# Optimization experiments

Measured on AMD Instinct MI355X. Metric: run time of the kernel, lower is better.

The kernel has to match this reference:

```python
import jax, jax.numpy as jnp
import numpy as np

B, L, D = 2, 2048, 2048
H, KV, HD = 16, 8, 128
EPS = 1e-5
ROPE_BASE = 10000.0
SCALING_ALPHA = 1.0
SCALE = HD ** -0.5


def setup_inputs() -> dict:
    key = jax.random.key(0)
    ks = jax.random.split(key, 5)
    s = 0.02  # weight init scale
    return {
        "x": jax.random.normal(ks[0], (B, L, D), jnp.float32),
        "wq": jax.random.normal(ks[1], (D, H * HD), jnp.float32) * s,
        "wk": jax.random.normal(ks[2], (D, KV * HD), jnp.float32) * s,
        "wv": jax.random.normal(ks[3], (D, KV * HD), jnp.float32) * s,
        "wo": jax.random.normal(ks[4], (H * HD, D), jnp.float32) * s,
        "qn_w": jnp.ones((HD,), jnp.float32),
        "kn_w": jnp.ones((HD,), jnp.float32),
    }


def _rope(t):
    # t: [B, h, L, HD]. DynamicNTKAlpha base scaling (alpha=1 -> no-op).
    base = ROPE_BASE * SCALING_ALPHA ** (HD / (HD - 2))
    # NOTE: source uses base**(+i/d) (no negative exponent) -- kept faithful.
    freqs = base ** (jnp.arange(0, HD, 2, dtype=jnp.float32) / HD)  # [HD/2]
    pos = jnp.arange(t.shape[-2], dtype=jnp.float32)                # [L]
    angles = pos[:, None] * freqs[None, :]                          # [L, HD/2]
    cos, sin = jnp.cos(angles), jnp.sin(angles)
    x1, x2 = t[..., : HD // 2], t[..., HD // 2 :]
    return jnp.concatenate([x1 * cos - x2 * sin, x2 * cos + x1 * sin], axis=-1)


def _rmsnorm(t, w):
    return t * jax.lax.rsqrt(jnp.mean(t * t, axis=-1, keepdims=True) + EPS) * w


def reference(x, wq, wk, wv, wo, qn_w, kn_w):
    b, l, _ = x.shape
    q = (x @ wq).reshape(b, l, H, HD).transpose(0, 2, 1, 3)   # [B,H,L,HD]
    k = (x @ wk).reshape(b, l, KV, HD).transpose(0, 2, 1, 3)  # [B,KV,L,HD]
    v = (x @ wv).reshape(b, l, KV, HD).transpose(0, 2, 1, 3)
    q = _rmsnorm(_rope(q), qn_w)
    k = _rmsnorm(_rope(k), kn_w)
    # GQA: expand KV heads to match query heads
    rep = H // KV
    k = jnp.repeat(k, rep, axis=1)  # [B,H,L,HD]
    v = jnp.repeat(v, rep, axis=1)
    scores = jnp.einsum("bhqd,bhkd->bhqk", q, k) * SCALE
    probs = jax.nn.softmax(scores, axis=-1)
    out = jnp.einsum("bhqk,bhkd->bhqd", probs, v)             # [B,H,L,HD]
    out = out.transpose(0, 2, 1, 3).reshape(b, l, H * HD)
    return out @ wo
```

## Files before the change

kernel.cpp:

```cpp
#include <hip/hip_runtime.h>
#include <math.h>

#define BB 2
#define LL 2048
#define DD 2048
#define HH 16
#define KVH 8
#define HDIM 128
#define SCALE_F 0.08838834764831845f
#define EPS_F 1e-5f
#define LOG2E 1.4426950408889634f
#define SMAX_F 17.0f
#define QKVW 4096

typedef unsigned short u16;
typedef __attribute__((ext_vector_type(8))) short short8;
typedef __attribute__((ext_vector_type(4))) float f32x4;

#define MFMA16(a, b, c) __builtin_amdgcn_mfma_f32_16x16x32_bf16((a), (b), (c), 0, 0, 0)

__device__ __forceinline__ float b2f(u16 u) {
    union { unsigned int i; float f; } x;
    x.i = ((unsigned int)u) << 16;
    return x.f;
}
__device__ __forceinline__ u16 f2b(float f) {
    unsigned int x = __float_as_uint(f);
    unsigned int r = x + 0x7FFFu + ((x >> 16) & 1u);
    return (u16)(r >> 16);
}
__device__ __forceinline__ u16 f2b_fast(float f) {
    return (u16)((__float_as_uint(f) + 0x8000u) >> 16);
}
__device__ __forceinline__ void g2l(const u16* g, u16* l) {
    __builtin_amdgcn_global_load_lds(
        (const __attribute__((address_space(1))) unsigned int*)g,
        (__attribute__((address_space(3))) unsigned int*)l, 16, 0, 0);
}

__global__ __launch_bounds__(256) void convert_f32_bf16(const float* __restrict__ in,
                                                        u16* __restrict__ out, int n) {
    int i = (blockIdx.x * 256 + threadIdx.x) * 4;
    if (i >= n) return;
    float4 v = *(const float4*)(in + i);
    unsigned int p0 = (unsigned int)f2b(v.x) | ((unsigned int)f2b(v.y) << 16);
    unsigned int p1 = (unsigned int)f2b(v.z) | ((unsigned int)f2b(v.w) << 16);
    uint2 pk; pk.x = p0; pk.y = p1;
    *(uint2*)(out + i) = pk;
}

__global__ __launch_bounds__(256) void transpose_conv(const float* __restrict__ in,
                                                      u16* __restrict__ out, int R, int C) {
    __shared__ u16 t[64 * 65];
    int c0 = blockIdx.x * 64, r0 = blockIdx.y * 64;
#pragma unroll
    for (int i = 0; i < 16; i++) {
        int idx = threadIdx.x + i * 256;
        int r = idx >> 6, c = idx & 63;
        t[r * 65 + c] = f2b(in[(size_t)(r0 + r) * C + c0 + c]);
    }
    __syncthreads();
#pragma unroll
    for (int i = 0; i < 16; i++) {
        int idx = threadIdx.x + i * 256;
        int r = idx >> 6, c = idx & 63;
        out[(size_t)(c0 + r) * R + r0 + c] = t[c * 65 + r];
    }
}

__global__ __launch_bounds__(256) void transpose_v(const u16* __restrict__ qkv,
                                                   u16* __restrict__ vt) {
    __shared__ u16 t[64 * 65];
    int l0 = blockIdx.x * 64, d0 = blockIdx.y * 64;
    int bg = blockIdx.z, b = bg >> 3, g = bg & 7;
    const u16* src = qkv + (size_t)b * LL * QKVW + 3072 + g * HDIM;
    u16* dst = vt + (size_t)bg * HDIM * LL;
#pragma unroll
    for (int i = 0; i < 16; i++) {
        int idx = threadIdx.x + i * 256;
        int r = idx >> 6, c = idx & 63;
        t[r * 65 + c] = src[(size_t)(l0 + r) * QKVW + d0 + c];
    }
    __syncthreads();
#pragma unroll
    for (int i = 0; i < 16; i++) {
        int idx = threadIdx.x + i * 256;
        int r = idx >> 6, c = idx & 63;
        dst[(size_t)(d0 + r) * LL + l0 + c] = t[c * 65 + r];
    }
}

__global__ __launch_bounds__(256) void rope_table(float* __restrict__ ct, float* __restrict__ st) {
    int i = blockIdx.x * 256 + threadIdx.x;
    int pos = i >> 6, d = i & 63;
    float freq = (float)pow(10000.0, (double)d * (1.0 / 64.0));
    float ang = (float)pos * freq;
    double a = (double)ang;
    ct[i] = (float)cos(a);
    st[i] = (float)sin(a);
}

template <bool F32OUT>
__global__ __launch_bounds__(256) void gemm_bt(const u16* __restrict__ A,
                                               const u16* __restrict__ Bt,
                                               void* __restrict__ Cv, int M, int N, int K) {
    __shared__ __align__(16) u16 As[128 * 32];
    __shared__ __align__(16) u16 Bs[128 * 32];
    const int tid = threadIdx.x;
    const int w = tid >> 6, lane = tid & 63;
    const int lm = lane & 15, lq = lane >> 4;
    const int bn0 = blockIdx.x * 128, bm0 = blockIdx.y * 128;
    const int wm = (w >> 1) * 64, wn = (w & 1) * 64;

    f32x4 acc[4][4];
#pragma unroll
    for (int i = 0; i < 4; i++)
#pragma unroll
        for (int j = 0; j < 4; j++) acc[i][j] = (f32x4){0.f, 0.f, 0.f, 0.f};

    const int sr = w * 32 + (lane >> 2);
    const int scc = lane & 3;
    const u16* ga = A + (size_t)(bm0 + sr) * K + scc * 8;
    const u16* gb = Bt + (size_t)(bn0 + sr) * K + scc * 8;
    u16* lA = &As[w * 1024];
    u16* lB = &Bs[w * 1024];

    for (int k0 = 0; k0 < K; k0 += 32) {
        __syncthreads();
        g2l(ga + k0, lA);
        g2l(ga + (size_t)16 * K + k0, lA + 512);
        g2l(gb + k0, lB);
        g2l(gb + (size_t)16 * K + k0, lB + 512);
        __syncthreads();

        short8 af[4], bf[4];
#pragma unroll
        for (int mt = 0; mt < 4; mt++)
            af[mt] = *(const short8*)(&As[(wm + mt * 16 + lm) * 32 + lq * 8]);
#pragma unroll
        for (int nt = 0; nt < 4; nt++)
            bf[nt] = *(const short8*)(&Bs[(wn + nt * 16 + lm) * 32 + lq * 8]);
#pragma unroll
        for (int mt = 0; mt < 4; mt++)
#pragma unroll
            for (int nt = 0; nt < 4; nt++) acc[mt][nt] = MFMA16(af[mt], bf[nt], acc[mt][nt]);
    }

#pragma unroll
    for (int mt = 0; mt < 4; mt++)
#pragma unroll
        for (int nt = 0; nt < 4; nt++)
#pragma unroll
            for (int r = 0; r < 4; r++) {
                int row = bm0 + wm + mt * 16 + lq * 4 + r;
                int col = bn0 + wn + nt * 16 + lm;
                if (F32OUT)
                    ((float*)Cv)[(size_t)row * N + col] = acc[mt][nt][r];
                else
                    ((u16*)Cv)[(size_t)row * N + col] = f2b(acc[mt][nt][r]);
            }
}

__global__ __launch_bounds__(256) void rope_norm(u16* __restrict__ qkv,
                                                 const float* __restrict__ qw,
                                                 const float* __restrict__ kw,
                                                 const float* __restrict__ ct,
                                                 const float* __restrict__ st) {
    int slot = blockIdx.x * 4 + (threadIdx.x >> 6);
    int lane = threadIdx.x & 63;
    int hh = slot % (HH + KVH);
    int row = slot / (HH + KVH);
    int pos = row & (LL - 1);

    u16* base = qkv + (size_t)row * QKVW + hh * HDIM;
    const float* w = (hh < HH) ? qw : kw;

    float x1 = b2f(base[lane]), x2 = b2f(base[lane + 64]);
    float c = ct[pos * 64 + lane], s = st[pos * 64 + lane];
    float r1 = x1 * c - x2 * s;
    float r2 = x2 * c + x1 * s;
    float ss = r1 * r1 + r2 * r2;
#pragma unroll
    for (int m = 1; m < 64; m <<= 1) ss += __shfl_xor(ss, m, 64);
    float sc = 1.0f / sqrtf(ss * (1.0f / 128.0f) + EPS_F);
    base[lane] = f2b(r1 * sc * w[lane]);
    base[lane + 64] = f2b(r2 * sc * w[lane + 64]);
}

__global__ __launch_bounds__(256, 4) void attn_kernel(const u16* __restrict__ qkv,
                                                      const u16* __restrict__ vt,
                                                      u16* __restrict__ ob) {
    __shared__ __align__(16) u16 Kt[64 * 128];
    __shared__ __align__(16) u16 Vt[128 * 64];
    __shared__ __align__(16) u16 Ps[64 * 64];

    const int tid = threadIdx.x, w = tid >> 6, lane = tid & 63;
    const int lm = lane & 15, lq = lane >> 4;
    const int q0 = blockIdx.x * 64;
    const int bh = blockIdx.y, b = bh >> 4, hd = bh & 15, g = hd >> 1;

    const u16* kbase = qkv + (size_t)b * LL * QKVW + 2048 + g * HDIM;
    const u16* vtbase = vt + (size_t)(b * KVH + g) * HDIM * LL;

    const int krl = lane >> 4, kgl = lane & 15;
    const int vrl = lane >> 3, vgl = lane & 7;

    short8 aq[4];
    {
        size_t qoff = (size_t)(b * LL + q0 + w * 16 + lm) * QKVW + hd * HDIM + lq * 8;
#pragma unroll
        for (int kk = 0; kk < 4; kk++) aq[kk] = *(const short8*)(qkv + qoff + kk * 32);
    }

    f32x4 o[8];
#pragma unroll
    for (int i = 0; i < 8; i++) o[i] = (f32x4){0.f, 0.f, 0.f, 0.f};
    float psum[4] = {0.f, 0.f, 0.f, 0.f};
    const float SC2 = SCALE_F * LOG2E;

    for (int t = 0; t < LL / 64; t++) {
        __syncthreads();
#pragma unroll
        for (int ch = 0; ch < 4; ch++) {
            int r = w * 16 + ch * 4 + krl;
            int gc = kgl ^ (r & 15);
            g2l(kbase + (size_t)(t * 64 + r) * QKVW + gc * 8,
                &Kt[(w * 16 + ch * 4) * 128]);
        }
#pragma unroll
        for (int ch = 0; ch < 4; ch++) {
            int r = w * 32 + ch * 8 + vrl;
            int gc = vgl ^ (r & 7);
            g2l(vtbase + (size_t)r * LL + t * 64 + gc * 8,
                &Vt[(w * 32 + ch * 8) * 64]);
        }
        __syncthreads();

        f32x4 s[4];
#pragma unroll
        for (int nt = 0; nt < 4; nt++) {
            s[nt] = (f32x4){0.f, 0.f, 0.f, 0.f};
#pragma unroll
            for (int kk = 0; kk < 4; kk++) {
                int gg = (kk * 4 + lq) ^ lm;
                short8 bf = *(const short8*)(&Kt[(nt * 16 + lm) * 128 + gg * 8]);
                s[nt] = MFMA16(aq[kk], bf, s[nt]);
            }
        }

#pragma unroll
        for (int nt = 0; nt < 4; nt++)
#pragma unroll
            for (int r = 0; r < 4; r++) {
                float p = exp2f(fmaf(s[nt][r], SC2, -SMAX_F));
                psum[r] += p;
                int row = lq * 4 + r;
                int keyx = (nt * 16 + lm) ^ ((row & 7) << 3);
                Ps[(w * 16 + row) * 64 + keyx] = f2b_fast(p);
            }

#pragma unroll
        for (int kk = 0; kk < 2; kk++) {
            int keyb = (kk * 32 + lq * 8) ^ ((lm & 7) << 3);
            short8 pa = *(const short8*)(&Ps[(w * 16 + lm) * 64 + keyb]);
#pragma unroll
            for (int dn = 0; dn < 8; dn++) {
                int gg = (kk * 4 + lq) ^ (lm & 7);
                short8 bv = *(const short8*)(&Vt[(dn * 16 + lm) * 64 + gg * 8]);
                o[dn] = MFMA16(pa, bv, o[dn]);
            }
        }
    }

#pragma unroll
    for (int m = 1; m < 16; m <<= 1)
#pragma unroll
        for (int r = 0; r < 4; r++) psum[r] += __shfl_xor(psum[r], m, 64);
    float inv[4];
#pragma unroll
    for (int r = 0; r < 4; r++) inv[r] = 1.0f / psum[r];

    size_t obase = (size_t)(b * LL + q0 + w * 16 + lq * 4) * (HH * HDIM) + hd * HDIM;
#pragma unroll
    for (int dn = 0; dn < 8; dn++)
#pragma unroll
        for (int r = 0; r < 4; r++)
            ob[obase + (size_t)r * (HH * HDIM) + dn * 16 + lm] = f2b(o[dn][r] * inv[r]);
}

extern "C" void kernel_launch(void* const* d_in, const int* in_sizes, int n_in,
                              void* d_out, int out_size, void* d_ws, size_t ws_size,
                              hipStream_t stream) {
    const float* x  = (const float*)d_in[0];
    const float* wq = (const float*)d_in[1];
    const float* wk = (const float*)d_in[2];
    const float* wv = (const float*)d_in[3];
    const float* wo = (const float*)d_in[4];
    const float* qn = (const float*)d_in[5];
    const float* kn = (const float*)d_in[6];

    u16* ws = (u16*)d_ws;
    const size_t SZ_X = (size_t)BB * LL * DD;
    u16* xb    = ws;
    u16* qkv   = xb + SZ_X;
    u16* wqkvT = qkv + (size_t)BB * LL * QKVW;
    u16* woT   = wqkvT + (size_t)QKVW * DD;
    float* ct  = (float*)(woT + (size_t)DD * DD);
    float* st  = ct + (size_t)LL * 64;
    u16* att = xb;
    u16* vt  = wqkvT;

    convert_f32_bf16<<<dim3((unsigned)(SZ_X / 1024)), dim3(256), 0, stream>>>(x, xb, (int)SZ_X);
    transpose_conv<<<dim3(32, 32), dim3(256), 0, stream>>>(wq, wqkvT, DD, DD);
    transpose_conv<<<dim3(16, 32), dim3(256), 0, stream>>>(wk, wqkvT + (size_t)2048 * DD, DD, KVH * HDIM);
    transpose_conv<<<dim3(16, 32), dim3(256), 0, stream>>>(wv, wqkvT + (size_t)3072 * DD, DD, KVH * HDIM);
    transpose_conv<<<dim3(32, 32), dim3(256), 0, stream>>>(wo, woT, HH * HDIM, DD);
    rope_table<<<dim3(LL * 64 / 256), dim3(256), 0, stream>>>(ct, st);

    gemm_bt<false><<<dim3(QKVW / 128, BB * LL / 128), dim3(256), 0, stream>>>(xb, wqkvT, qkv, BB * LL, QKVW, DD);

    rope_norm<<<dim3(BB * LL * (HH + KVH) / 4), dim3(256), 0, stream>>>(qkv, qn, kn, ct, st);
    transpose_v<<<dim3(LL / 64, HDIM / 64, BB * KVH), dim3(256), 0, stream>>>(qkv, vt);

    attn_kernel<<<dim3(LL / 64, BB * HH), dim3(256), 0, stream>>>(qkv, vt, att);
    gemm_bt<true><<<dim3(DD / 128, BB * LL / 128), dim3(256), 0, stream>>>(att, woT, d_out, BB * LL, DD, DD);
}
```

Measured before the change: 414.7 us.

## Switch attention to 32x32 MFMA tiles with 128 query rows per block

Rewrites the attention kernel to use 32x32x16 bf16 MFMA instructions, with each wave handling 32 query rows and each block 128 rows. This doubles the reuse of each K/V tile loaded into shared memory and reduces the number of LDS reads per MFMA. In exchange it uses more registers (launch bounds lowered to 2 blocks per CU), halves the grid size and adds an extra block barrier per key tile.

```diff
diff --git a/kernel.cpp b/kernel.cpp
--- a/kernel.cpp
+++ b/kernel.cpp
@@ -16,8 +16,10 @@
 typedef unsigned short u16;
 typedef __attribute__((ext_vector_type(8))) short short8;
 typedef __attribute__((ext_vector_type(4))) float f32x4;
+typedef __attribute__((ext_vector_type(16))) float f32x16;
 
 #define MFMA16(a, b, c) __builtin_amdgcn_mfma_f32_16x16x32_bf16((a), (b), (c), 0, 0, 0)
+#define MFMA32(a, b, c) __builtin_amdgcn_mfma_f32_32x32x16_bf16((a), (b), (c), 0, 0, 0)
 
 __device__ __forceinline__ float b2f(u16 u) {
     union { unsigned int i; float f; } x;
@@ -187,16 +189,16 @@
     base[lane + 64] = f2b(r2 * sc * w[lane + 64]);
 }
 
-__global__ __launch_bounds__(256, 4) void attn_kernel(const u16* __restrict__ qkv,
+__global__ __launch_bounds__(256, 2) void attn_kernel(const u16* __restrict__ qkv,
                                                       const u16* __restrict__ vt,
                                                       u16* __restrict__ ob) {
     __shared__ __align__(16) u16 Kt[64 * 128];
     __shared__ __align__(16) u16 Vt[128 * 64];
-    __shared__ __align__(16) u16 Ps[64 * 64];
+    __shared__ __align__(16) u16 Ps[4][32 * 64];
 
     const int tid = threadIdx.x, w = tid >> 6, lane = tid & 63;
-    const int lm = lane & 15, lq = lane >> 4;
-    const int q0 = blockIdx.x * 64;
+    const int l31 = lane & 31, lh = lane >> 5;
+    const int q0 = blockIdx.x * 128;
     const int bh = blockIdx.y, b = bh >> 4, hd = bh & 15, g = hd >> 1;
 
     const u16* kbase = qkv + (size_t)b * LL * QKVW + 2048 + g * HDIM;
@@ -205,17 +207,22 @@
     const int krl = lane >> 4, kgl = lane & 15;
     const int vrl = lane >> 3, vgl = lane & 7;
 
-    short8 aq[4];
+    const int qrow = q0 + w * 32 + l31;
+    short8 aq[8];
     {
-        size_t qoff = (size_t)(b * LL + q0 + w * 16 + lm) * QKVW + hd * HDIM + lq * 8;
-#pragma unroll
-        for (int kk = 0; kk < 4; kk++) aq[kk] = *(const short8*)(qkv + qoff + kk * 32);
-    }
-
-    f32x4 o[8];
-#pragma unroll
-    for (int i = 0; i < 8; i++) o[i] = (f32x4){0.f, 0.f, 0.f, 0.f};
-    float psum[4] = {0.f, 0.f, 0.f, 0.f};
+        const u16* qp = qkv + (size_t)(b * LL + qrow) * QKVW + hd * HDIM + lh * 8;
+#pragma unroll
+        for (int kk = 0; kk < 8; kk++) aq[kk] = *(const short8*)(qp + kk * 16);
+    }
+
+    f32x16 o[4];
+#pragma unroll
+    for (int i = 0; i < 4; i++)
+#pragma unroll
+        for (int r = 0; r < 16; r++) o[i][r] = 0.f;
+    float psum[16];
+#pragma unroll
+    for (int r = 0; r < 16; r++) psum[r] = 0.f;
     const float SC2 = SCALE_F * LOG2E;
 
     for (int t = 0; t < LL / 64; t++) {
@@ -236,56 +243,63 @@
         }
         __syncthreads();
 
-        f32x4 s[4];
-#pragma unroll
-        for (int nt = 0; nt < 4; nt++) {
-            s[nt] = (f32x4){0.f, 0.f, 0.f, 0.f};
-#pragma unroll
-            for (int kk = 0; kk < 4; kk++) {
-                int gg = (kk * 4 + lq) ^ lm;
-                short8 bf = *(const short8*)(&Kt[(nt * 16 + lm) * 128 + gg * 8]);
-                s[nt] = MFMA16(aq[kk], bf, s[nt]);
+        f32x16 s[2];
+#pragma unroll
+        for (int kt = 0; kt < 2; kt++) {
+#pragma unroll
+            for (int r = 0; r < 16; r++) s[kt][r] = 0.f;
+            int key = kt * 32 + l31;
+#pragma unroll
+            for (int kk = 0; kk < 8; kk++) {
+                int gg = (kk * 2 + lh) ^ (key & 15);
+                short8 bf = *(const short8*)(&Kt[key * 128 + gg * 8]);
+                s[kt] = MFMA32(aq[kk], bf, s[kt]);
             }
         }
 
 #pragma unroll
-        for (int nt = 0; nt < 4; nt++)
-#pragma unroll
-            for (int r = 0; r < 4; r++) {
-                float p = exp2f(fmaf(s[nt][r], SC2, -SMAX_F));
+        for (int kt = 0; kt < 2; kt++) {
+            int key = kt * 32 + l31;
+#pragma unroll
+            for (int r = 0; r < 16; r++) {
+                float p = exp2f(fmaf(s[kt][r], SC2, -SMAX_F));
                 psum[r] += p;
-                int row = lq * 4 + r;
-                int keyx = (nt * 16 + lm) ^ ((row & 7) << 3);
-                Ps[(w * 16 + row) * 64 + keyx] = f2b_fast(p);
+                int row = (r & 3) + 8 * (r >> 2) + 4 * lh;
+                Ps[w][row * 64 + (key ^ ((row & 7) << 3))] = f2b_fast(p);
             }
-
-#pragma unroll
-        for (int kk = 0; kk < 2; kk++) {
-            int keyb = (kk * 32 + lq * 8) ^ ((lm & 7) << 3);
-            short8 pa = *(const short8*)(&Ps[(w * 16 + lm) * 64 + keyb]);
-#pragma unroll
-            for (int dn = 0; dn < 8; dn++) {
-                int gg = (kk * 4 + lq) ^ (lm & 7);
-                short8 bv = *(const short8*)(&Vt[(dn * 16 + lm) * 64 + gg * 8]);
-                o[dn] = MFMA16(pa, bv, o[dn]);
+        }
+        __syncthreads();
+
+#pragma unroll
+        for (int kc = 0; kc < 4; kc++) {
+            int gp = ((kc * 2 + lh) ^ (l31 & 7)) * 8;
+            short8 pa = *(const short8*)(&Ps[w][l31 * 64 + gp]);
+#pragma unroll
+            for (int dn = 0; dn < 4; dn++) {
+                int d = dn * 32 + l31;
+                int gv = ((kc * 2 + lh) ^ (d & 7)) * 8;
+                short8 bv = *(const short8*)(&Vt[d * 64 + gv]);
+                o[dn] = MFMA32(pa, bv, o[dn]);
             }
         }
     }
 
 #pragma unroll
-    for (int m = 1; m < 16; m <<= 1)
-#pragma unroll
-        for (int r = 0; r < 4; r++) psum[r] += __shfl_xor(psum[r], m, 64);
-    float inv[4];
-#pragma unroll
-    for (int r = 0; r < 4; r++) inv[r] = 1.0f / psum[r];
-
-    size_t obase = (size_t)(b * LL + q0 + w * 16 + lq * 4) * (HH * HDIM) + hd * HDIM;
-#pragma unroll
-    for (int dn = 0; dn < 8; dn++)
-#pragma unroll
-        for (int r = 0; r < 4; r++)
-            ob[obase + (size_t)r * (HH * HDIM) + dn * 16 + lm] = f2b(o[dn][r] * inv[r]);
+    for (int m = 1; m < 32; m <<= 1)
+#pragma unroll
+        for (int r = 0; r < 16; r++) psum[r] += __shfl_xor(psum[r], m, 32);
+    float inv[16];
+#pragma unroll
+    for (int r = 0; r < 16; r++) inv[r] = 1.0f / psum[r];
+
+    u16* obase = ob + (size_t)(b * LL + q0 + w * 32) * (HH * HDIM) + hd * HDIM;
+#pragma unroll
+    for (int dn = 0; dn < 4; dn++)
+#pragma unroll
+        for (int r = 0; r < 16; r++) {
+            int row = (r & 3) + 8 * (r >> 2) + 4 * lh;
+            obase[(size_t)row * (HH * HDIM) + dn * 32 + l31] = f2b(o[dn][r] * inv[r]);
+        }
 }
 
 extern "C" void kernel_launch(void* const* d_in, const int* in_sizes, int n_in,
@@ -322,6 +336,6 @@
     rope_norm<<<dim3(BB * LL * (HH + KVH) / 4), dim3(256), 0, stream>>>(qkv, qn, kn, ct, st);
     transpose_v<<<dim3(LL / 64, HDIM / 64, BB * KVH), dim3(256), 0, stream>>>(qkv, vt);
 
-    attn_kernel<<<dim3(LL / 64, BB * HH), dim3(256), 0, stream>>>(qkv, vt, att);
+    attn_kernel<<<dim3(LL / 128, BB * HH), dim3(256), 0, stream>>>(qkv, vt, att);
     gemm_bt<true><<<dim3(DD / 128, BB * LL / 128), dim3(256), 0, stream>>>(att, woT, d_out, BB * LL, DD, DD);
 }
```

Measured after the change: 412.2 us. About the same (-0.6%).
